# Kernel tuning notes

Hardware: AMD Instinct MI355X
Metric: run time of the kernel (lower is better)

## Reference

```python
import jax, jax.numpy as jnp
import numpy as np

B, N, K = 32, 1024, 20          # graphs, points per graph, kNN neighbors
EMB = 1024                       # emb_dims
OUT = 7                          # out_channels
WS1, ST1, G1 = 52, 20, 7         # linear1 STFT-KAN: window, stride, gridsize
WS2, ST2, G2 = 197, 7, 6         # linear2 STFT-KAN
NW1 = (128 - WS1) // ST1 + 1     # 4 windows over 128-dim features
NW2 = (2 * EMB - WS2) // ST2 + 1 # 265 windows over 2048-dim features


def _window(kind, M):
    n = jnp.arange(M, dtype=jnp.float32)
    if kind == 'bartlett':
        return 1.0 - jnp.abs(2.0 * n / M - 1.0)        # periodic bartlett (torch default)
    return 0.5 * (1.0 - jnp.cos(2.0 * jnp.pi * n / M)) # periodic hann


def _stft_kan(x, coeffs, bias, gridsize, ws, stride, wtype):
    """x: [B, D]; coeffs: [2, outdim, nw, ws, gridsize]; returns [B, outdim]."""
    D = x.shape[1]
    nw = (D - ws) // stride + 1
    idx = jnp.arange(nw)[:, None] * stride + jnp.arange(ws)[None, :]  # [nw, ws]
    xw = x[:, idx] * _window(wtype, ws)                               # [B, nw, ws]
    kk = jnp.arange(1, gridsize + 1, dtype=x.dtype)
    ang = xw[..., None] * kk                                          # [B, nw, ws, g]
    y = jnp.einsum('bnwg,onwg->bo', jnp.cos(ang), coeffs[0])
    y = y + jnp.einsum('bnwg,onwg->bo', jnp.sin(ang), coeffs[1])
    return y + bias


def setup_inputs() -> dict:
    key = jax.random.key(0)
    ks = jax.random.split(key, 8)
    pos = jax.random.normal(ks[0], (B * N, 3), jnp.float32)
    batch = jnp.repeat(jnp.arange(B, dtype=jnp.int32), N)  # sorted, equal-size graphs
    # EdgeConv MLP([6,64,128]): Linear+BN+ReLU, then plain Linear
    W1 = jax.random.normal(ks[1], (6, 64), jnp.float32) * 0.3
    b1 = jnp.zeros((64,), jnp.float32)
    gamma1 = jnp.ones((64,), jnp.float32)
    beta1 = jnp.zeros((64,), jnp.float32)
    W2 = jax.random.normal(ks[2], (64, 128), jnp.float32) * 0.1
    b2 = jnp.zeros((128,), jnp.float32)
    # STFT-KAN 1 (smooth init: coeffs damped by k^2)
    k1 = np.arange(1, G1 + 1, dtype=np.float32)
    c1 = jax.random.normal(ks[3], (2, EMB, NW1, WS1, G1), jnp.float32) / (np.sqrt(NW1 * WS1) * (k1 ** 2))
    bi1 = jnp.zeros((EMB,), jnp.float32)
    # STFT-KAN 2 (non-smooth init)
    c2 = jax.random.normal(ks[4], (2, OUT, NW2, WS2, G2), jnp.float32) / (np.sqrt(NW2 * WS2) * np.sqrt(G2))
    bi2 = jnp.zeros((OUT,), jnp.float32)
    return {"pos": pos, "batch": batch, "W1": W1, "b1": b1, "gamma1": gamma1,
            "beta1": beta1, "W2": W2, "b2": b2, "c1": c1, "bi1": bi1, "c2": c2, "bi2": bi2}


def reference(pos, batch, W1, b1, gamma1, beta1, W2, b2, c1, bi1, c2, bi2):
    p = pos.reshape(B, N, 3)
    # dynamic kNN graph per batch element (exclude self)
    sq = jnp.sum(p * p, axis=-1)                                    # [B, N]
    d2 = sq[:, :, None] + sq[:, None, :] - 2.0 * jnp.einsum('bnd,bmd->bnm', p, p)
    d2 = d2 + jnp.eye(N, dtype=p.dtype) * 1e10
    _, idx = jax.lax.top_k(-d2, K)                                  # [B, N, K]
    pj = jax.vmap(lambda pts, ids: pts[ids])(p, idx)                # [B, N, K, 3]
    pi = jnp.broadcast_to(p[:, :, None, :], (B, N, K, 3))
    e = jnp.concatenate([pi, pj - pi], axis=-1)                     # [B, N, K, 6]
    # edge MLP: Linear -> BN -> ReLU -> Linear
    h = e @ W1 + b1
    mu = h.mean((0, 1, 2))
    var = h.var((0, 1, 2))
    h = gamma1 * (h - mu) * jax.lax.rsqrt(var + 1e-5) + beta1
    h = jax.nn.relu(h)
    h = h @ W2 + b2                                                 # [B, N, K, 128]
    x1 = h.max(axis=2).reshape(B * N, 128)                          # max aggregation over neighbors
    x = _stft_kan(x1, c1, bi1, G1, WS1, ST1, 'bartlett')            # [B*N, EMB]
    xg = x.reshape(B, N, EMB)
    xcat = jnp.concatenate([xg.max(axis=1), xg.mean(axis=1)], axis=-1)  # global max/mean pool
    return _stft_kan(xcat, c2, bi2, G2, WS2, ST2, 'hann')           # [B, OUT]
```

## Files before the change

kernel.cpp:

```cpp
#include <hip/hip_runtime.h>
#include <cstdint>

typedef _Float16 half8 __attribute__((ext_vector_type(8)));
typedef float f32x4 __attribute__((ext_vector_type(4)));

__device__ __forceinline__ void gload16(const void* g, void* l) {
  __builtin_amdgcn_global_load_lds(
      (const __attribute__((address_space(1))) void*)g,
      (__attribute__((address_space(3))) void*)l, 16, 0, 0);
}

__global__ __launch_bounds__(256) void knn_kernel(const float* __restrict__ pos,
                                                  int* __restrict__ nbr) {
  __shared__ float px[1024], py[1024], pz[1024], sq[1024];
  int tid = threadIdx.x;
  int b = blockIdx.x >> 8;
  const float* pg = pos + (size_t)b * 3072;
  for (int m = 0; m < 4; ++m) {
    int j = m * 256 + tid;
    float x = pg[3 * j], y = pg[3 * j + 1], z = pg[3 * j + 2];
    px[j] = x; py[j] = y; pz[j] = z; sq[j] = x * x + y * y + z * z;
  }
  __syncthreads();
  int wave = tid >> 6, lane = tid & 63;
  int n = (blockIdx.x & 255) * 4 + wave;
  float xi = px[n], yi = py[n], zi = pz[n], si = sq[n];
  float d[16];
#pragma unroll
  for (int i = 0; i < 16; ++i) {
    int j = i * 64 + lane;
    float dd = si + sq[j] - 2.0f * (xi * px[j] + yi * py[j] + zi * pz[j]);
    d[i] = (j == n) ? 1e30f : dd;
  }
  int outbase = (b * 1024 + n) * 20;
  for (int kk = 0; kk < 20; ++kk) {
    float lmin = d[0]; int lpos = 0;
#pragma unroll
    for (int i = 1; i < 16; ++i)
      if (d[i] < lmin) { lmin = d[i]; lpos = i; }
    float bv = lmin; int bi = lpos * 64 + lane;
#pragma unroll
    for (int off = 1; off < 64; off <<= 1) {
      float ov = __shfl_xor(bv, off);
      int   oi = __shfl_xor(bi, off);
      if (ov < bv || (ov == bv && oi < bi)) { bv = ov; bi = oi; }
    }
    if (lane == 0) nbr[outbase + kk] = b * 1024 + bi;
    if ((bi & 63) == lane) {
      int rp = bi >> 6;
#pragma unroll
      for (int i = 0; i < 16; ++i)
        if (i == rp) d[i] = 1e30f;
    }
  }
}

__global__ __launch_bounds__(256) void edge_stats_kernel(
    const float* __restrict__ pos, const int* __restrict__ nbr,
    const float* __restrict__ W1, const float* __restrict__ b1v,
    float* __restrict__ psum, float* __restrict__ psq) {
  __shared__ float els[256][6];
  __shared__ float w1s[384];
  __shared__ float b1s[64];
  __shared__ float red[8][64];
  int tid = threadIdx.x, bid = blockIdx.x;
  for (int f = tid; f < 384; f += 256) w1s[f] = W1[f];
  if (tid < 64) b1s[tid] = b1v[tid];
  int c = tid & 63, grp = tid >> 6;
  float s = 0.f, s2 = 0.f;
  for (int ch = 0; ch < 5; ++ch) {
    int E = bid * 1280 + ch * 256 + tid;
    int p = E / 20;
    int j = nbr[E];
    float pix = pos[3 * p], piy = pos[3 * p + 1], piz = pos[3 * p + 2];
    float e3 = pos[3 * j] - pix, e4 = pos[3 * j + 1] - piy, e5 = pos[3 * j + 2] - piz;
    __syncthreads();
    els[tid][0] = pix; els[tid][1] = piy; els[tid][2] = piz;
    els[tid][3] = e3;  els[tid][4] = e4;  els[tid][5] = e5;
    __syncthreads();
    for (int m = 0; m < 64; ++m) {
      int e = grp * 64 + m;
      float h = b1s[c];
#pragma unroll
      for (int d = 0; d < 6; ++d) h += els[e][d] * w1s[d * 64 + c];
      s += h; s2 += h * h;
    }
  }
  red[grp][c] = s;
  __syncthreads();
  red[4 + grp][c] = s2;
  __syncthreads();
  if (tid < 64) {
    float S = red[0][tid] + red[1][tid] + red[2][tid] + red[3][tid];
    float Q = red[4][tid] + red[5][tid] + red[6][tid] + red[7][tid];
    psum[bid * 64 + tid] = S;
    psq[bid * 64 + tid] = Q;
  }
}

__global__ void bn_finalize_kernel(const float* __restrict__ psum, const float* __restrict__ psq,
                                   const float* __restrict__ gamma, const float* __restrict__ beta,
                                   float* __restrict__ bns, float* __restrict__ bnh) {
  int c = threadIdx.x;
  float s = 0.f, q = 0.f;
  for (int b = 0; b < 512; ++b) { s += psum[b * 64 + c]; q += psq[b * 64 + c]; }
  const float inv = 1.0f / 655360.0f;
  float mu = s * inv;
  float var = q * inv - mu * mu;
  float sc = gamma[c] * rsqrtf(var + 1e-5f);
  bns[c] = sc;
  bnh[c] = beta[c] - mu * sc;
}

__global__ __launch_bounds__(256) void edge_mlp_kernel(
    const float* __restrict__ pos, const int* __restrict__ nbr,
    const float* __restrict__ W1, const float* __restrict__ b1v,
    const float* __restrict__ bns, const float* __restrict__ bnh,
    const float* __restrict__ W2, const float* __restrict__ b2v,
    float* __restrict__ x1) {
  __shared__ __align__(16) char elds[53248];
  _Float16* Ah = (_Float16*)(elds);
  _Float16* Al = (_Float16*)(elds + 10240);
  _Float16* Bh = (_Float16*)(elds + 20480);
  _Float16* Bl = (_Float16*)(elds + 36864);
  float* outb = (float*)elds;
  __shared__ float w1s[384];
  __shared__ float b1s[64], scs[64], shs[64];
  int tid = threadIdx.x, bid = blockIdx.x;
  for (int f = tid; f < 384; f += 256) w1s[f] = W1[f];
  if (tid < 64) { b1s[tid] = b1v[tid]; scs[tid] = bns[tid]; shs[tid] = bnh[tid]; }
#pragma unroll
  for (int i = 0; i < 32; ++i) {
    int flat = tid + 256 * i;
    int dd = flat >> 7, c = flat & 127;
    float v = W2[flat];
    _Float16 hi = (_Float16)v;
    _Float16 lo = (_Float16)(v - (float)hi);
    int byte = c * 128 + ((((dd >> 3) ^ (c & 7))) << 4) + (dd & 7) * 2;
    *(_Float16*)((char*)Bh + byte) = hi;
    *(_Float16*)((char*)Bl + byte) = lo;
  }
  __syncthreads();
#pragma unroll
  for (int m = 0; m < 20; ++m) {
    int flat = tid + 256 * m;
    int row = flat >> 6;
    int d = flat & 63;
    int j = nbr[bid * 80 + row];
    int P = bid * 4 + (row / 20);
    float pix = pos[3 * P], piy = pos[3 * P + 1], piz = pos[3 * P + 2];
    float e3 = pos[3 * j] - pix, e4 = pos[3 * j + 1] - piy, e5 = pos[3 * j + 2] - piz;
    float h = b1s[d];
    h += pix * w1s[d] + piy * w1s[64 + d] + piz * w1s[128 + d]
       + e3 * w1s[192 + d] + e4 * w1s[256 + d] + e5 * w1s[320 + d];
    h = scs[d] * h + shs[d];
    h = fmaxf(h, 0.f);
    _Float16 hi = (_Float16)h;
    _Float16 lo = (_Float16)(h - (float)hi);
    int byte = row * 128 + ((((d >> 3) ^ (row & 7))) << 4) + (d & 7) * 2;
    *(_Float16*)((char*)Ah + byte) = hi;
    *(_Float16*)((char*)Al + byte) = lo;
  }
  __syncthreads();
  int wave = tid >> 6, lane = tid & 63;
  int l15 = lane & 15, l4 = lane >> 4;
  f32x4 acc[5][2] = {};
#pragma unroll
  for (int ks = 0; ks < 2; ++ks) {
    int slotk = ks * 4 + l4;
    half8 bfh[2], bfl[2];
#pragma unroll
    for (int ci = 0; ci < 2; ++ci) {
      int col = (wave * 2 + ci) * 16 + l15;
      int byte = col * 128 + ((slotk ^ (col & 7)) << 4);
      bfh[ci] = *(const half8*)((char*)Bh + byte);
      bfl[ci] = *(const half8*)((char*)Bl + byte);
    }
#pragma unroll
    for (int rt = 0; rt < 5; ++rt) {
      int row = rt * 16 + l15;
      int byte = row * 128 + ((slotk ^ (row & 7)) << 4);
      half8 ah = *(const half8*)((char*)Ah + byte);
      half8 al = *(const half8*)((char*)Al + byte);
#pragma unroll
      for (int ci = 0; ci < 2; ++ci) {
        acc[rt][ci] = __builtin_amdgcn_mfma_f32_16x16x32_f16(ah, bfh[ci], acc[rt][ci], 0, 0, 0);
        acc[rt][ci] = __builtin_amdgcn_mfma_f32_16x16x32_f16(ah, bfl[ci], acc[rt][ci], 0, 0, 0);
        acc[rt][ci] = __builtin_amdgcn_mfma_f32_16x16x32_f16(al, bfh[ci], acc[rt][ci], 0, 0, 0);
      }
    }
  }
  __syncthreads();
#pragma unroll
  for (int rt = 0; rt < 5; ++rt)
#pragma unroll
    for (int ci = 0; ci < 2; ++ci) {
      int col = (wave * 2 + ci) * 16 + l15;
#pragma unroll
      for (int q = 0; q < 4; ++q) {
        int row = rt * 16 + l4 * 4 + q;
        outb[row * 129 + col] = acc[rt][ci][q];
      }
    }
  __syncthreads();
#pragma unroll
  for (int r = 0; r < 2; ++r) {
    int it = tid + 256 * r;
    int p = it >> 7, c = it & 127;
    float mx = -1e30f;
#pragma unroll
    for (int e = 0; e < 20; ++e) mx = fmaxf(mx, outb[(p * 20 + e) * 129 + c]);
    x1[((size_t)bid * 4 + p) * 128 + c] = mx + b2v[c];
  }
}

__global__ void c1_to_f16_kernel(const float* __restrict__ c1, _Float16* __restrict__ Cf) {
  int L = blockIdx.x * 256 + threadIdx.x;
  if (L >= 1024 * 3328) return;
  int o = L / 3328, rem = L % 3328;
  int w = rem >> 6, idx = rem & 63;
  int s = idx >> 3, e = idx & 7;
  int phase = s >> 2, n = s & 3;
  float v = 0.0f;
  if (e < 7)
    v = c1[((((size_t)phase * 1024 + o) * 4 + n) * 52 + w) * 7 + e];
  Cf[L] = (_Float16)v;
}

__global__ __launch_bounds__(512, 2) void kan1_gemm_kernel(
    const float* __restrict__ x1, const _Float16* __restrict__ Cf,
    float* __restrict__ pmax, float* __restrict__ psump) {
  __shared__ __align__(16) float xs[128 * 112];
  __shared__ __align__(16) _Float16 Asm[2][128 * 64];
  __shared__ __align__(16) _Float16 Bsm[2][256 * 64];
  int tid = threadIdx.x;
  int bm = blockIdx.x, bn = blockIdx.y;
  int m0 = bm << 7, n0 = bn << 8;
  int wave = tid >> 6, lane = tid & 63;
  int wr = wave >> 2, wc = wave & 3;
  int l15 = lane & 15, l4 = lane >> 4;

  auto stageB = [&](int t, int nb) {
    int j0 = t << 6;
#pragma unroll
    for (int i = 0; i < 4; ++i) {
      int idx = i * 512 + tid;
      int col = idx >> 3, slot = idx & 7;
      int sslot = slot ^ (col & 7);
      gload16(Cf + (size_t)(n0 + col) * 3328 + j0 + sslot * 8,
              (char*)Bsm[nb] + idx * 16);
    }
  };
  int sA = tid & 7;
  int phA = sA >> 2, nA = sA & 3;
  auto agen = [&](int t, int nb) {
    float bart = 1.0f - fabsf((float)(2 * t) * (1.0f / 52.0f) - 1.0f);
    int d = nA * 20 + t;
#pragma unroll
    for (int rep = 0; rep < 2; ++rep) {
      int r = (tid >> 3) + rep * 64;
      float th = xs[r * 112 + d] * bart;
      float sn, cs;
      __sincosf(th, &sn, &cs);
      float c2 = 2.0f * cs;
      float p0 = phA ? sn : cs;
      float p1 = phA ? c2 * sn : c2 * cs - 1.0f;
      half8 av;
      av[0] = (_Float16)p0; av[1] = (_Float16)p1;
      float pm2 = p0, pm1 = p1;
#pragma unroll
      for (int g = 2; g < 7; ++g) {
        float pg = c2 * pm1 - pm2;
        av[g] = (_Float16)pg;
        pm2 = pm1; pm1 = pg;
      }
      av[7] = (_Float16)0.0f;
      *(half8*)((char*)Asm[nb] + r * 128 + ((sA ^ (r & 7)) << 4)) = av;
    }
  };

#pragma unroll
  for (int i = 0; i < 7; ++i) {
    int idx = i * 512 + tid;
    int f = idx * 4;
    int row = f / 112, col = f - row * 112;
    gload16(x1 + (size_t)(m0 + row) * 128 + col, (char*)xs + idx * 16);
  }
  stageB(0, 0);
  f32x4 acc[4][4] = {};
  __syncthreads();
  agen(0, 0);
  __syncthreads();

  for (int t = 0; t < 52; ++t) {
    int cur = t & 1, nxt = cur ^ 1;
    if (t < 51) stageB(t + 1, nxt);
    half8 af[2][4], bf[2][4];
#pragma unroll
    for (int ksub = 0; ksub < 2; ++ksub) {
      int slotk = ksub * 4 + l4;
#pragma unroll
      for (int mi = 0; mi < 4; ++mi) {
        int row = wr * 64 + mi * 16 + l15;
        af[ksub][mi] = *(const half8*)((char*)Asm[cur] + row * 128 + ((slotk ^ (row & 7)) << 4));
      }
#pragma unroll
      for (int ni = 0; ni < 4; ++ni) {
        int col = wc * 64 + ni * 16 + l15;
        bf[ksub][ni] = *(const half8*)((char*)Bsm[cur] + col * 128 + ((slotk ^ (col & 7)) << 4));
      }
    }
    if (t < 51) agen(t + 1, nxt);
#pragma unroll
    for (int ksub = 0; ksub < 2; ++ksub)
#pragma unroll
      for (int mi = 0; mi < 4; ++mi)
#pragma unroll
        for (int ni = 0; ni < 4; ++ni)
          acc[mi][ni] = __builtin_amdgcn_mfma_f32_16x16x32_f16(af[ksub][mi], bf[ksub][ni], acc[mi][ni], 0, 0, 0);
    __syncthreads();
  }

  float* pooled = (float*)xs;
#pragma unroll
  for (int ni = 0; ni < 4; ++ni) {
    float mx = -1e30f, sm = 0.f;
#pragma unroll
    for (int mi = 0; mi < 4; ++mi)
#pragma unroll
      for (int q = 0; q < 4; ++q) {
        float v = acc[mi][ni][q];
        mx = fmaxf(mx, v); sm += v;
      }
    mx = fmaxf(mx, __shfl_xor(mx, 16)); sm += __shfl_xor(sm, 16);
    mx = fmaxf(mx, __shfl_xor(mx, 32)); sm += __shfl_xor(sm, 32);
    if (l4 == 0) {
      int col = wc * 64 + ni * 16 + l15;
      pooled[(wr * 2 + 0) * 256 + col] = mx;
      pooled[(wr * 2 + 1) * 256 + col] = sm;
    }
  }
  __syncthreads();
  if (tid < 256) {
    float mx = fmaxf(pooled[tid], pooled[512 + tid]);
    float sm = pooled[256 + tid] + pooled[768 + tid];
    pmax[(size_t)bm * 1024 + n0 + tid] = mx;
    psump[(size_t)bm * 1024 + n0 + tid] = sm;
  }
}

__global__ void pool_reduce_kernel(const float* __restrict__ pmax, const float* __restrict__ psump,
                                   const float* __restrict__ bi1,
                                   float* __restrict__ gmax, float* __restrict__ gmean) {
  int gid = blockIdx.x * 256 + threadIdx.x;
  int b = gid >> 10, col = gid & 1023;
  float mx = -1e30f, sm = 0.f;
  for (int t = 0; t < 8; ++t) {
    mx = fmaxf(mx, pmax[(size_t)(b * 8 + t) * 1024 + col]);
    sm += psump[(size_t)(b * 8 + t) * 1024 + col];
  }
  float bias = bi1[col];
  gmax[gid] = mx + bias;
  gmean[gid] = sm * (1.0f / 1024.0f) + bias;
}

__global__ __launch_bounds__(256) void kan2_kernel(
    const float* __restrict__ gmax, const float* __restrict__ gmean,
    const float* __restrict__ c2, float* __restrict__ part) {
  __shared__ float xc[2048];
  __shared__ float hw[197];
  __shared__ float racc[7][256];
  int b = blockIdx.x, s = blockIdx.y, tid = threadIdx.x;
  for (int f = tid; f < 1024; f += 256) {
    xc[f] = gmax[b * 1024 + f];
    xc[1024 + f] = gmean[b * 1024 + f];
  }
  for (int f = tid; f < 197; f += 256)
    hw[f] = 0.5f * (1.0f - cosf(6.283185307179586f * (float)f / 197.0f));
  float acc[7] = {};
  __syncthreads();
  int qlo = (52205 * s) / 16, qhi = (52205 * (s + 1)) / 16;
  for (int q = qlo + tid; q < qhi; q += 256) {
    int n = q / 197;
    int w = q - n * 197;
    float xw = xc[n * 7 + w] * hw[w];
    float s1, c1v;
    __sincosf(xw, &s1, &c1v);
    float ckv[6], skv[6];
    {
      float ck = c1v, sk = s1;
#pragma unroll
      for (int g = 0; g < 6; ++g) {
        ckv[g] = ck; skv[g] = sk;
        float cn = ck * c1v - sk * s1;
        sk = sk * c1v + ck * s1;
        ck = cn;
      }
    }
    int base = q * 6;
#pragma unroll
    for (int o = 0; o < 7; ++o) {
      const float* pc = c2 + (size_t)o * 313230 + base;
      const float* ps = c2 + (size_t)(o + 7) * 313230 + base;
      float sc = 0.f, ss = 0.f;
#pragma unroll
      for (int g = 0; g < 6; ++g) { sc += ckv[g] * pc[g]; ss += skv[g] * ps[g]; }
      acc[o] += sc + ss;
    }
  }
#pragma unroll
  for (int o = 0; o < 7; ++o) racc[o][tid] = acc[o];
  __syncthreads();
  for (int st = 128; st >= 1; st >>= 1) {
    if (tid < st)
#pragma unroll
      for (int o = 0; o < 7; ++o) racc[o][tid] += racc[o][tid + st];
    __syncthreads();
  }
  if (tid < 7) part[(b * 16 + s) * 7 + tid] = racc[tid][0];
}

__global__ void kan2_reduce_kernel(const float* __restrict__ part, const float* __restrict__ bi2,
                                   float* __restrict__ out) {
  int i = threadIdx.x;
  if (i >= 224) return;
  int b = i / 7, o = i % 7;
  float s = 0.f;
  for (int t = 0; t < 16; ++t) s += part[(b * 16 + t) * 7 + o];
  out[b * 7 + o] = s + bi2[o];
}

extern "C" void kernel_launch(void* const* d_in, const int* in_sizes, int n_in,
                              void* d_out, int out_size, void* d_ws, size_t ws_size,
                              hipStream_t stream) {
  const float* pos    = (const float*)d_in[0];
  const float* W1     = (const float*)d_in[2];
  const float* b1     = (const float*)d_in[3];
  const float* gamma1 = (const float*)d_in[4];
  const float* beta1  = (const float*)d_in[5];
  const float* W2     = (const float*)d_in[6];
  const float* b2     = (const float*)d_in[7];
  const float* c1     = (const float*)d_in[8];
  const float* bi1    = (const float*)d_in[9];
  const float* c2     = (const float*)d_in[10];
  const float* bi2    = (const float*)d_in[11];
  float* out = (float*)d_out;
  char* ws = (char*)d_ws;

  int*      nbr   = (int*)     (ws + 0);
  float*    x1    = (float*)   (ws + 2621440);
  _Float16* Cf    = (_Float16*)(ws + 19398656);
  float*    psum  = (float*)   (ws + 26214400);
  float*    psq   = (float*)   (ws + 26345472);
  float*    bns   = (float*)   (ws + 26476544);
  float*    bnh   = (float*)   (ws + 26476800);
  float*    pmax  = (float*)   (ws + 26477056);
  float*    psump = (float*)   (ws + 27525632);
  float*    gmax  = (float*)   (ws + 28574208);
  float*    gmean = (float*)   (ws + 28705280);
  float*    part  = (float*)   (ws + 28836352);
  if (ws_size < 28850688) return;

  knn_kernel<<<8192, 256, 0, stream>>>(pos, nbr);
  c1_to_f16_kernel<<<13312, 256, 0, stream>>>(c1, Cf);
  edge_stats_kernel<<<512, 256, 0, stream>>>(pos, nbr, W1, b1, psum, psq);
  bn_finalize_kernel<<<1, 64, 0, stream>>>(psum, psq, gamma1, beta1, bns, bnh);
  edge_mlp_kernel<<<8192, 256, 0, stream>>>(pos, nbr, W1, b1, bns, bnh, W2, b2, x1);
  kan1_gemm_kernel<<<dim3(256, 4), 512, 0, stream>>>(x1, Cf, pmax, psump);
  pool_reduce_kernel<<<128, 256, 0, stream>>>(pmax, psump, bi1, gmax, gmean);
  kan2_kernel<<<dim3(32, 16), 256, 0, stream>>>(gmax, gmean, c2, part);
  kan2_reduce_kernel<<<1, 256, 0, stream>>>(part, bi2, out);
}
```

Measured before the change: 592.9 us.

## Generate KAN1 A-operand in registers and retile GEMM to 256x128 blocks

The KAN1 GEMM no longer stages x1 and the cos/sin Chebyshev-recurrence A tiles through shared memory. Each lane now loads its own x values and builds the MFMA A fragments directly in registers, split into cosine and sine halves. The block tile changes from 128x256 to 256x128, which halves the B-tile LDS footprint and raises launch bounds to 4 blocks per SM for occupancy. The cost is redundant sincos work across the waves that share rows, plus per-iteration global loads of x. Pool partials and workspace offsets are adjusted to match.

```diff
diff --git a/kernel.cpp b/kernel.cpp
--- a/kernel.cpp
+++ b/kernel.cpp
@@ -227,23 +227,21 @@
   Cf[L] = (_Float16)v;
 }
 
-__global__ __launch_bounds__(512, 2) void kan1_gemm_kernel(
+__global__ __launch_bounds__(512, 4) void kan1_gemm_kernel(
     const float* __restrict__ x1, const _Float16* __restrict__ Cf,
     float* __restrict__ pmax, float* __restrict__ psump) {
-  __shared__ __align__(16) float xs[128 * 112];
-  __shared__ __align__(16) _Float16 Asm[2][128 * 64];
-  __shared__ __align__(16) _Float16 Bsm[2][256 * 64];
+  __shared__ __align__(16) _Float16 Bsm[2][128 * 64];
   int tid = threadIdx.x;
   int bm = blockIdx.x, bn = blockIdx.y;
-  int m0 = bm << 7, n0 = bn << 8;
+  int m0 = bm << 8, n0 = bn << 7;
   int wave = tid >> 6, lane = tid & 63;
-  int wr = wave >> 2, wc = wave & 3;
+  int wr = wave >> 1, wc = wave & 1;
   int l15 = lane & 15, l4 = lane >> 4;
 
   auto stageB = [&](int t, int nb) {
     int j0 = t << 6;
 #pragma unroll
-    for (int i = 0; i < 4; ++i) {
+    for (int i = 0; i < 2; ++i) {
       int idx = i * 512 + tid;
       int col = idx >> 3, slot = idx & 7;
       int sslot = slot ^ (col & 7);
@@ -251,77 +249,72 @@
               (char*)Bsm[nb] + idx * 16);
     }
   };
-  int sA = tid & 7;
-  int phA = sA >> 2, nA = sA & 3;
-  auto agen = [&](int t, int nb) {
+
+  const float* xbase = x1 + (size_t)(m0 + wr * 64 + l15) * 128 + l4 * 20;
+  float xr[4];
+#pragma unroll
+  for (int mi = 0; mi < 4; ++mi) xr[mi] = xbase[mi * 2048];
+  stageB(0, 0);
+  f32x4 acc[4][4] = {};
+  __syncthreads();
+
+  for (int t = 0; t < 52; ++t) {
+    int cur = t & 1, nxt = cur ^ 1;
+    if (t < 51) stageB(t + 1, nxt);
     float bart = 1.0f - fabsf((float)(2 * t) * (1.0f / 52.0f) - 1.0f);
-    int d = nA * 20 + t;
-#pragma unroll
-    for (int rep = 0; rep < 2; ++rep) {
-      int r = (tid >> 3) + rep * 64;
-      float th = xs[r * 112 + d] * bart;
+    half8 a0[4], a1[4];
+#pragma unroll
+    for (int mi = 0; mi < 4; ++mi) {
+      float th = xr[mi] * bart;
       float sn, cs;
       __sincosf(th, &sn, &cs);
       float c2 = 2.0f * cs;
-      float p0 = phA ? sn : cs;
-      float p1 = phA ? c2 * sn : c2 * cs - 1.0f;
-      half8 av;
-      av[0] = (_Float16)p0; av[1] = (_Float16)p1;
-      float pm2 = p0, pm1 = p1;
-#pragma unroll
-      for (int g = 2; g < 7; ++g) {
-        float pg = c2 * pm1 - pm2;
-        av[g] = (_Float16)pg;
-        pm2 = pm1; pm1 = pg;
-      }
-      av[7] = (_Float16)0.0f;
-      *(half8*)((char*)Asm[nb] + r * 128 + ((sA ^ (r & 7)) << 4)) = av;
-    }
-  };
-
-#pragma unroll
-  for (int i = 0; i < 7; ++i) {
-    int idx = i * 512 + tid;
-    int f = idx * 4;
-    int row = f / 112, col = f - row * 112;
-    gload16(x1 + (size_t)(m0 + row) * 128 + col, (char*)xs + idx * 16);
-  }
-  stageB(0, 0);
-  f32x4 acc[4][4] = {};
-  __syncthreads();
-  agen(0, 0);
-  __syncthreads();
-
-  for (int t = 0; t < 52; ++t) {
-    int cur = t & 1, nxt = cur ^ 1;
-    if (t < 51) stageB(t + 1, nxt);
-    half8 af[2][4], bf[2][4];
-#pragma unroll
-    for (int ksub = 0; ksub < 2; ++ksub) {
-      int slotk = ksub * 4 + l4;
-#pragma unroll
-      for (int mi = 0; mi < 4; ++mi) {
-        int row = wr * 64 + mi * 16 + l15;
-        af[ksub][mi] = *(const half8*)((char*)Asm[cur] + row * 128 + ((slotk ^ (row & 7)) << 4));
-      }
+      float cp2 = cs, cp1 = c2 * cs - 1.0f;
+      float sp2 = sn, sp1 = c2 * sn;
+      a0[mi][0] = (_Float16)cp2; a0[mi][1] = (_Float16)cp1;
+      a1[mi][0] = (_Float16)sp2; a1[mi][1] = (_Float16)sp1;
+#pragma unroll
+      for (int e = 2; e < 7; ++e) {
+        float cn = c2 * cp1 - cp2; cp2 = cp1; cp1 = cn;
+        float sv = c2 * sp1 - sp2; sp2 = sp1; sp1 = sv;
+        a0[mi][e] = (_Float16)cn; a1[mi][e] = (_Float16)sv;
+      }
+      a0[mi][7] = (_Float16)0.0f; a1[mi][7] = (_Float16)0.0f;
+    }
+    if (t < 51) {
+#pragma unroll
+      for (int mi = 0; mi < 4; ++mi) xr[mi] = xbase[mi * 2048 + t + 1];
+    }
+    {
+      half8 bf[4];
 #pragma unroll
       for (int ni = 0; ni < 4; ++ni) {
         int col = wc * 64 + ni * 16 + l15;
-        bf[ksub][ni] = *(const half8*)((char*)Bsm[cur] + col * 128 + ((slotk ^ (col & 7)) << 4));
-      }
-    }
-    if (t < 51) agen(t + 1, nxt);
-#pragma unroll
-    for (int ksub = 0; ksub < 2; ++ksub)
+        bf[ni] = *(const half8*)((char*)Bsm[cur] + col * 128 + ((l4 ^ (col & 7)) << 4));
+      }
 #pragma unroll
       for (int mi = 0; mi < 4; ++mi)
 #pragma unroll
         for (int ni = 0; ni < 4; ++ni)
-          acc[mi][ni] = __builtin_amdgcn_mfma_f32_16x16x32_f16(af[ksub][mi], bf[ksub][ni], acc[mi][ni], 0, 0, 0);
+          acc[mi][ni] = __builtin_amdgcn_mfma_f32_16x16x32_f16(a0[mi], bf[ni], acc[mi][ni], 0, 0, 0);
+    }
+    {
+      half8 bf[4];
+#pragma unroll
+      for (int ni = 0; ni < 4; ++ni) {
+        int col = wc * 64 + ni * 16 + l15;
+        bf[ni] = *(const half8*)((char*)Bsm[cur] + col * 128 + (((4 + l4) ^ (col & 7)) << 4));
+      }
+#pragma unroll
+      for (int mi = 0; mi < 4; ++mi)
+#pragma unroll
+        for (int ni = 0; ni < 4; ++ni)
+          acc[mi][ni] = __builtin_amdgcn_mfma_f32_16x16x32_f16(a1[mi], bf[ni], acc[mi][ni], 0, 0, 0);
+    }
     __syncthreads();
   }
 
-  float* pooled = (float*)xs;
+  float* pooled = (float*)Bsm;
 #pragma unroll
   for (int ni = 0; ni < 4; ++ni) {
     float mx = -1e30f, sm = 0.f;
@@ -336,14 +329,18 @@
     mx = fmaxf(mx, __shfl_xor(mx, 32)); sm += __shfl_xor(sm, 32);
     if (l4 == 0) {
       int col = wc * 64 + ni * 16 + l15;
-      pooled[(wr * 2 + 0) * 256 + col] = mx;
-      pooled[(wr * 2 + 1) * 256 + col] = sm;
-    }
-  }
-  __syncthreads();
-  if (tid < 256) {
-    float mx = fmaxf(pooled[tid], pooled[512 + tid]);
-    float sm = pooled[256 + tid] + pooled[768 + tid];
+      pooled[(wr * 2 + 0) * 128 + col] = mx;
+      pooled[(wr * 2 + 1) * 128 + col] = sm;
+    }
+  }
+  __syncthreads();
+  if (tid < 128) {
+    float mx = pooled[tid], sm = pooled[128 + tid];
+#pragma unroll
+    for (int w = 1; w < 4; ++w) {
+      mx = fmaxf(mx, pooled[(w * 2 + 0) * 128 + tid]);
+      sm += pooled[(w * 2 + 1) * 128 + tid];
+    }
     pmax[(size_t)bm * 1024 + n0 + tid] = mx;
     psump[(size_t)bm * 1024 + n0 + tid] = sm;
   }
@@ -355,9 +352,9 @@
   int gid = blockIdx.x * 256 + threadIdx.x;
   int b = gid >> 10, col = gid & 1023;
   float mx = -1e30f, sm = 0.f;
-  for (int t = 0; t < 8; ++t) {
-    mx = fmaxf(mx, pmax[(size_t)(b * 8 + t) * 1024 + col]);
-    sm += psump[(size_t)(b * 8 + t) * 1024 + col];
+  for (int t = 0; t < 4; ++t) {
+    mx = fmaxf(mx, pmax[(size_t)(b * 4 + t) * 1024 + col]);
+    sm += psump[(size_t)(b * 4 + t) * 1024 + col];
   }
   float bias = bi1[col];
   gmax[gid] = mx + bias;
@@ -455,18 +452,18 @@
   float*    bns   = (float*)   (ws + 26476544);
   float*    bnh   = (float*)   (ws + 26476800);
   float*    pmax  = (float*)   (ws + 26477056);
-  float*    psump = (float*)   (ws + 27525632);
-  float*    gmax  = (float*)   (ws + 28574208);
-  float*    gmean = (float*)   (ws + 28705280);
-  float*    part  = (float*)   (ws + 28836352);
-  if (ws_size < 28850688) return;
+  float*    psump = (float*)   (ws + 27001344);
+  float*    gmax  = (float*)   (ws + 27525632);
+  float*    gmean = (float*)   (ws + 27656704);
+  float*    part  = (float*)   (ws + 27787776);
+  if (ws_size < 27802112) return;
 
   knn_kernel<<<8192, 256, 0, stream>>>(pos, nbr);
   c1_to_f16_kernel<<<13312, 256, 0, stream>>>(c1, Cf);
   edge_stats_kernel<<<512, 256, 0, stream>>>(pos, nbr, W1, b1, psum, psq);
   bn_finalize_kernel<<<1, 64, 0, stream>>>(psum, psq, gamma1, beta1, bns, bnh);
   edge_mlp_kernel<<<8192, 256, 0, stream>>>(pos, nbr, W1, b1, bns, bnh, W2, b2, x1);
-  kan1_gemm_kernel<<<dim3(256, 4), 512, 0, stream>>>(x1, Cf, pmax, psump);
+  kan1_gemm_kernel<<<dim3(128, 8), 512, 0, stream>>>(x1, Cf, pmax, psump);
   pool_reduce_kernel<<<128, 256, 0, stream>>>(pmax, psump, bi1, gmax, gmean);
   kan2_kernel<<<dim3(32, 16), 256, 0, stream>>>(gmax, gmean, c2, part);
   kan2_reduce_kernel<<<1, 256, 0, stream>>>(part, bi2, out);
```

Result: slower. 604.9 us (+2.0%).
